# Performance work log

Hardware: AMD Instinct MI355X
Metric: run time of the kernel (lower is better)

The kernel has to match this reference:

```python
import jax, jax.numpy as jnp
import numpy as np

D_MODEL = 1024
NUM_HEADS = 16
D_K = D_MODEL // NUM_HEADS
THETA = 10000.0
B, S = 4, 2048


def apply_rope(x, positions):
    # x: [b, h, s, d_k]; positions: [b, s] int. Interleaved-pair RoPE (cs336 style).
    half = D_K // 2
    inv_freq = THETA ** (-jnp.arange(half, dtype=jnp.float32) * 2.0 / D_K)  # [half]
    ang = positions.astype(jnp.float32)[..., None] * inv_freq  # [b, s, half]
    cos = jnp.cos(ang)[:, None, :, :]  # [b, 1, s, half]
    sin = jnp.sin(ang)[:, None, :, :]
    x_even = x[..., 0::2]
    x_odd = x[..., 1::2]
    r_even = x_even * cos - x_odd * sin
    r_odd = x_even * sin + x_odd * cos
    out = jnp.stack([r_even, r_odd], axis=-1)  # [b,h,s,half,2]
    return out.reshape(x.shape)


def setup_inputs() -> dict:
    key = jax.random.key(0)
    ks = jax.random.split(key, 5)
    scale = 1.0 / np.sqrt(D_MODEL)
    x = jax.random.normal(ks[0], (B, S, D_MODEL), dtype=jnp.float32)
    Qw = jax.random.normal(ks[1], (D_MODEL, D_MODEL), dtype=jnp.float32) * scale
    Kw = jax.random.normal(ks[2], (D_MODEL, D_MODEL), dtype=jnp.float32) * scale
    Vw = jax.random.normal(ks[3], (D_MODEL, D_MODEL), dtype=jnp.float32) * scale
    Ow = jax.random.normal(ks[4], (D_MODEL, D_MODEL), dtype=jnp.float32) * scale
    token_positions = jnp.broadcast_to(jnp.arange(S, dtype=jnp.int32), (B, S))
    return {"x": x, "token_positions": token_positions, "Qw": Qw, "Kw": Kw, "Vw": Vw, "Ow": Ow}


def reference(x, token_positions, Qw, Kw, Vw, Ow):
    b, s, _ = x.shape
    # Projections: einsum('da db, ...sdb -> ...sda') == x @ W.T
    q = jnp.einsum('ab,bsb2->bsa', Qw, x, optimize=True) if False else x @ Qw.T
    k = x @ Kw.T
    v = x @ Vw.T
    # split heads: [b, s, h*dk] -> [b, h, s, dk]
    def split(t):
        return t.reshape(b, s, NUM_HEADS, D_K).transpose(0, 2, 1, 3)
    q, k, v = split(q), split(k), split(v)
    q = apply_rope(q, token_positions)
    k = apply_rope(k, token_positions)
    scores = jnp.einsum('bhqd,bhkd->bhqk', q, k) / jnp.sqrt(jnp.float32(D_K))
    causal = jnp.tril(jnp.ones((s, s), dtype=bool))  # triu(...).T == tril
    scores = jnp.where(causal, scores, jnp.float32(-1e30))
    attn = jax.nn.softmax(scores, axis=-1)
    out = jnp.einsum('bhqk,bhkd->bhqd', attn, v)
    out = out.transpose(0, 2, 1, 3).reshape(b, s, D_MODEL)
    return out @ Ow.T
```

## Files before the change

kernel.cpp:

```cpp
#include <hip/hip_runtime.h>

typedef __attribute__((ext_vector_type(4))) float f32x4;
typedef __attribute__((ext_vector_type(8))) short short8;
typedef __attribute__((ext_vector_type(2))) unsigned short ushort2v;
typedef __attribute__((ext_vector_type(4))) unsigned short ushort4v;

#define D_MODEL 1024
#define NH 16
#define DK 64
#define BSZ 4
#define SSZ 2048
#define M_TOT (BSZ * SSZ)

__device__ __forceinline__ unsigned short f2bf(float f) {
  unsigned int u = __float_as_uint(f);
  u = (u + 0x7FFFu + ((u >> 16) & 1u)) >> 16;
  return (unsigned short)u;
}
__device__ __forceinline__ float bf2f(unsigned short h) {
  return __uint_as_float(((unsigned int)h) << 16);
}
__device__ __forceinline__ unsigned int pk_bf16(float lo, float hi) {
  unsigned int r;
  asm("v_cvt_pk_bf16_f32 %0, %1, %2" : "=v"(r) : "v"(lo), "v"(hi));
  return r;
}
__device__ __forceinline__ float fast_exp2(float x) {
  float r;
  asm("v_exp_f32 %0, %1" : "=v"(r) : "v"(x));
  return r;
}

__global__ void convert_kernel(const float* __restrict__ x,
                               const float* __restrict__ Qw,
                               const float* __restrict__ Kw,
                               const float* __restrict__ Vw,
                               const float* __restrict__ Ow,
                               unsigned short* __restrict__ xb,
                               unsigned short* __restrict__ wqkv,
                               unsigned short* __restrict__ owb) {
  const int NX = M_TOT * D_MODEL;
  const int NO = D_MODEL * D_MODEL;
  const int NW = 3 * NO;
  int idx = (blockIdx.x * blockDim.x + threadIdx.x) * 4;
  const float* src;
  unsigned short* dst;
  if (idx < NX) {
    src = x + idx; dst = xb + idx;
  } else if (idx < NX + NW) {
    int j = idx - NX;
    dst = wqkv + j;
    if (j < NO)            src = Qw + j;
    else if (j < 2 * NO)   src = Kw + (j - NO);
    else                   src = Vw + (j - 2 * NO);
  } else {
    int j = idx - NX - NW;
    src = Ow + j; dst = owb + j;
  }
  float4 v = *(const float4*)src;
  ushort4v o;
  o.x = f2bf(v.x); o.y = f2bf(v.y); o.z = f2bf(v.z); o.w = f2bf(v.w);
  *(ushort4v*)dst = o;
}

template <int MODE>
__global__ __launch_bounds__(256) void gemm_kernel(const unsigned short* __restrict__ A,
                                                   const unsigned short* __restrict__ Bm,
                                                   unsigned short* __restrict__ oQ,
                                                   unsigned short* __restrict__ oK,
                                                   unsigned short* __restrict__ oV,
                                                   float* __restrict__ oF) {
  __shared__ unsigned short As[128 * 32];
  __shared__ unsigned short Bs[128 * 32];
  const int t = threadIdx.x;
  const int lane = t & 63, wave = t >> 6;
  const int l15 = lane & 15, g = lane >> 4;
  const int wr = wave >> 1, wc = wave & 1;
  const int brow = blockIdx.x * 128;
  const int bcol = blockIdx.y * 128;
  const int rA = t >> 2, c8 = (t & 3) * 8;

  f32x4 acc[4][4] = {};

  for (int k0 = 0; k0 < 1024; k0 += 32) {
    __syncthreads();
#pragma unroll
    for (int i = 0; i < 2; ++i) {
      const unsigned short* sa = A + (size_t)(brow + rA + 64 * i) * 1024 + k0 + c8;
      __builtin_amdgcn_global_load_lds((const __attribute__((address_space(1))) void*)sa,
                                       (__attribute__((address_space(3))) void*)(&As[(t + 256 * i) * 8]),
                                       16, 0, 0);
      const unsigned short* sb = Bm + (size_t)(bcol + rA + 64 * i) * 1024 + k0 + c8;
      __builtin_amdgcn_global_load_lds((const __attribute__((address_space(1))) void*)sb,
                                       (__attribute__((address_space(3))) void*)(&Bs[(t + 256 * i) * 8]),
                                       16, 0, 0);
    }
    __syncthreads();
    short8 a[4], b[4];
#pragma unroll
    for (int m = 0; m < 4; ++m)
      a[m] = *(const short8*)(&As[(wr * 64 + m * 16 + l15) * 32 + g * 8]);
#pragma unroll
    for (int n = 0; n < 4; ++n)
      b[n] = *(const short8*)(&Bs[(wc * 64 + n * 16 + l15) * 32 + g * 8]);
#pragma unroll
    for (int m = 0; m < 4; ++m)
#pragma unroll
      for (int n = 0; n < 4; ++n)
        acc[m][n] = __builtin_amdgcn_mfma_f32_16x16x32_bf16(a[m], b[n], acc[m][n], 0, 0, 0);
  }

  const int mbase = brow + wr * 64;
  const int nbase = bcol + wc * 64;
  if (MODE == 0) {
    const int which = bcol >> 10;
#pragma unroll
    for (int m = 0; m < 4; ++m) {
#pragma unroll
      for (int n = 0; n < 4; ++n) {
#pragma unroll
        for (int r = 0; r < 4; ++r) {
          int mrow = mbase + m * 16 + g * 4 + r;
          int ncol = nbase + n * 16 + l15;
          int b = mrow >> 11, s = mrow & 2047;
          int rem = ncol & 1023;
          int h = rem >> 6, d = rem & 63;
          int bh = b * NH + h;
          unsigned short val = f2bf(acc[m][n][r]);
          if (which == 0)      oQ[((size_t)bh * SSZ + s) * DK + d] = val;
          else if (which == 1) oK[((size_t)bh * SSZ + s) * DK + d] = val;
          else                 oV[((size_t)bh * DK + d) * SSZ + s] = val;
        }
      }
    }
  } else {
#pragma unroll
    for (int m = 0; m < 4; ++m) {
#pragma unroll
      for (int n = 0; n < 4; ++n) {
#pragma unroll
        for (int r = 0; r < 4; ++r) {
          int mrow = mbase + m * 16 + g * 4 + r;
          int ncol = nbase + n * 16 + l15;
          oF[(size_t)mrow * D_MODEL + ncol] = acc[m][n][r];
        }
      }
    }
  }
}

__global__ void rope_kernel(unsigned short* __restrict__ Qb,
                            unsigned short* __restrict__ Kb,
                            const int* __restrict__ pos) {
  int idx = blockIdx.x * blockDim.x + threadIdx.x;
  int i = idx & 31;
  int s = (idx >> 5) & (SSZ - 1);
  int bh = idx >> 16;
  int b = bh >> 4;
  float p = (float)pos[b * SSZ + s];
  const float KC = 0.28782313662425572f;
  float invf = expf(-KC * (float)i);
  float ang = p * invf;
  float sn, cs;
  sincosf(ang, &sn, &cs);
  size_t off = ((size_t)bh * SSZ + s) * DK + 2 * i;

  const float QS = 0.18033688011112042f;
  ushort2v q = *(ushort2v*)(Qb + off);
  float qe = bf2f(q.x), qo = bf2f(q.y);
  float re = (qe * cs - qo * sn) * QS;
  float ro = (qe * sn + qo * cs) * QS;
  q.x = f2bf(re); q.y = f2bf(ro);
  *(ushort2v*)(Qb + off) = q;

  ushort2v k = *(ushort2v*)(Kb + off);
  float ke = bf2f(k.x), ko = bf2f(k.y);
  float rke = ke * cs - ko * sn;
  float rko = ke * sn + ko * cs;
  k.x = f2bf(rke); k.y = f2bf(rko);
  *(ushort2v*)(Kb + off) = k;
}

__global__ __launch_bounds__(512) void attn_kernel(const unsigned short* __restrict__ Qb,
                                                   const unsigned short* __restrict__ Kb,
                                                   const unsigned short* __restrict__ Vt,
                                                   unsigned short* __restrict__ Ob) {
  __shared__ unsigned short KS[2][4096];
  __shared__ unsigned short VS[2][4096];
  __shared__ unsigned short PL[8 * 1024];
  const int id = blockIdx.x;
  const int xcd = id & 7, j = id >> 3;
  const int bh = 8 * xcd + (j & 7);
  const int bx = j >> 3;
  const int t = threadIdx.x;
  const int lane = t & 63, wave = t >> 6;
  const int l15 = lane & 15, g = lane >> 4;
  const size_t bhS = (size_t)bh * SSZ;
  char* plb = (char*)PL + wave * 2048;
  const int swz = (l15 & 7) << 4;
  const int b = bh >> 4, h = bh & 15;

  const int sr = t >> 3, ss = (t & 7) ^ (sr & 7);
  auto stage = [&](int bb, int j0) {
    const unsigned short* ks = Kb + (bhS + j0 + sr) * DK + ss * 8;
    __builtin_amdgcn_global_load_lds((const __attribute__((address_space(1))) void*)ks,
                                     (__attribute__((address_space(3))) void*)(&KS[bb][t * 8]),
                                     16, 0, 0);
    const unsigned short* vs = Vt + ((size_t)bh * DK + sr) * SSZ + j0 + ss * 8;
    __builtin_amdgcn_global_load_lds((const __attribute__((address_space(1))) void*)vs,
                                     (__attribute__((address_space(3))) void*)(&VS[bb][t * 8]),
                                     16, 0, 0);
  };

#pragma unroll 1
  for (int half = 0; half < 2; ++half) {
    const int qt = half ? (15 - bx) : bx;
    const int qw0 = qt * 128 + wave * 16;
    short8 qf[2];
#pragma unroll
    for (int ds = 0; ds < 2; ++ds)
      qf[ds] = *(const short8*)(Qb + (bhS + qw0 + l15) * DK + ds * 32 + g * 8);

    f32x4 acc[4] = {};
    float mrun = -3.0e38f, lrun = 0.f;
    const int njt = 2 * (qt + 1);

    int cur = 0;
    stage(0, 0);
    __syncthreads();

#pragma unroll 1
    for (int jt = 0; jt < njt; ++jt) {
      const int j0 = jt * 64;
      if (jt + 1 < njt) stage(cur ^ 1, j0 + 64);

      const unsigned short* Kc = KS[cur];
      short8 kf[4][2];
#pragma unroll
      for (int c = 0; c < 4; ++c)
#pragma unroll
        for (int ds = 0; ds < 2; ++ds)
          kf[c][ds] = *(const short8*)(Kc + (c * 16 + l15) * 64 + (((ds * 4 + g) ^ (l15 & 7)) * 8));

      f32x4 st[4] = {};
#pragma unroll
      for (int c = 0; c < 4; ++c)
#pragma unroll
        for (int ds = 0; ds < 2; ++ds)
          st[c] = __builtin_amdgcn_mfma_f32_16x16x32_bf16(kf[c][ds], qf[ds], st[c], 0, 0, 0);

      if (j0 + 64 > qw0) {
        const int qrow = qw0 + l15;
#pragma unroll
        for (int c = 0; c < 4; ++c) {
          const int kbse = j0 + c * 16 + g * 4;
#pragma unroll
          for (int r = 0; r < 4; ++r)
            if (kbse + r > qrow) st[c][r] = -3.0e38f;
        }
      }

      float mc[4];
#pragma unroll
      for (int c = 0; c < 4; ++c)
        mc[c] = fmaxf(fmaxf(st[c][0], st[c][1]), fmaxf(st[c][2], st[c][3]));
      float pmax = fmaxf(fmaxf(mc[0], mc[1]), fmaxf(mc[2], mc[3]));

      if (!__all(pmax <= mrun + 8.0f)) {
        float mx = fmaxf(pmax, __shfl_xor(pmax, 16));
        mx = fmaxf(mx, __shfl_xor(mx, 32));
        const float mnew = fmaxf(mrun, mx);
        const float corr = fast_exp2(mrun - mnew);
        mrun = mnew;
        lrun *= corr;
#pragma unroll
        for (int n = 0; n < 4; ++n)
#pragma unroll
          for (int r = 0; r < 4; ++r) acc[n][r] *= corr;
      }

      float sc_[4];
#pragma unroll
      for (int c = 0; c < 4; ++c) {
#pragma unroll
        for (int r = 0; r < 4; ++r)
          st[c][r] = fast_exp2(st[c][r] - mrun);
        sc_[c] = (st[c][0] + st[c][1]) + (st[c][2] + st[c][3]);
      }
      lrun += (sc_[0] + sc_[1]) + (sc_[2] + sc_[3]);

#pragma unroll
      for (int c = 0; c < 4; ++c) {
        uint2 ww;
        ww.x = pk_bf16(st[c][0], st[c][1]);
        ww.y = pk_bf16(st[c][2], st[c][3]);
        *(uint2*)(plb + ((l15 * 128 + c * 32 + g * 8) ^ swz)) = ww;
      }
      asm volatile("s_waitcnt lgkmcnt(0)" ::: "memory");
      __builtin_amdgcn_sched_barrier(0);
      short8 pf[2];
#pragma unroll
      for (int d2 = 0; d2 < 2; ++d2)
        pf[d2] = *(const short8*)(plb + ((l15 * 128 + d2 * 64 + g * 16) ^ swz));

      const unsigned short* Vc = VS[cur];
#pragma unroll
      for (int n = 0; n < 4; ++n) {
#pragma unroll
        for (int d2 = 0; d2 < 2; ++d2) {
          short8 vf = *(const short8*)(Vc + (n * 16 + l15) * 64 + (((d2 * 4 + g) ^ (l15 & 7)) * 8));
          acc[n] = __builtin_amdgcn_mfma_f32_16x16x32_bf16(vf, pf[d2], acc[n], 0, 0, 0);
        }
      }

      __syncthreads();
      cur ^= 1;
    }

    lrun += __shfl_xor(lrun, 16);
    lrun += __shfl_xor(lrun, 32);
    const float inv = 1.f / lrun;
    const size_t base = ((size_t)b * SSZ + qw0 + l15) * D_MODEL + h * DK;
#pragma unroll
    for (int n = 0; n < 4; ++n) {
      uint2 ww;
      ww.x = pk_bf16(acc[n][0] * inv, acc[n][1] * inv);
      ww.y = pk_bf16(acc[n][2] * inv, acc[n][3] * inv);
      *(uint2*)((char*)(Ob + base + n * 16 + g * 4)) = ww;
    }
    __syncthreads();
  }
}

extern "C" void kernel_launch(void* const* d_in, const int* in_sizes, int n_in,
                              void* d_out, int out_size, void* d_ws, size_t ws_size,
                              hipStream_t stream) {
  const float* x  = (const float*)d_in[0];
  const int* pos  = (const int*)d_in[1];
  const float* Qw = (const float*)d_in[2];
  const float* Kw = (const float*)d_in[3];
  const float* Vw = (const float*)d_in[4];
  const float* Ow = (const float*)d_in[5];
  float* out = (float*)d_out;

  unsigned short* xb   = (unsigned short*)d_ws;
  unsigned short* wqkv = xb + (size_t)M_TOT * D_MODEL;
  unsigned short* owb  = wqkv + (size_t)3 * D_MODEL * D_MODEL;
  unsigned short* Qb   = owb + (size_t)D_MODEL * D_MODEL;
  unsigned short* Kb   = Qb + (size_t)64 * SSZ * DK;
  unsigned short* Vt   = Kb + (size_t)64 * SSZ * DK;
  unsigned short* Ob   = Vt + (size_t)64 * SSZ * DK;

  {
    int total = M_TOT * D_MODEL + 4 * D_MODEL * D_MODEL;
    convert_kernel<<<total / 4 / 256, 256, 0, stream>>>(x, Qw, Kw, Vw, Ow, xb, wqkv, owb);
  }
  gemm_kernel<0><<<dim3(M_TOT / 128, 3072 / 128), 256, 0, stream>>>(xb, wqkv, Qb, Kb, Vt, nullptr);
  rope_kernel<<<(64 * SSZ * 32) / 256, 256, 0, stream>>>(Qb, Kb, pos);
  attn_kernel<<<512, 512, 0, stream>>>(Qb, Kb, Vt, Ob);
  gemm_kernel<1><<<dim3(M_TOT / 128, D_MODEL / 128), 256, 0, stream>>>(Ob, owb, nullptr, nullptr, nullptr, out);
}
```

Measured before the change: 280.8 us.

## Swizzle GEMM LDS tiles and stage V transpose through LDS for coalesced stores

Applies an XOR swizzle to the 16-byte chunk placement in the A/B LDS tiles, so that MFMA operand reads by lanes in the same wave fall in different banks. For the V output of the QKV projection, which is stored transposed, each wave now packs bf16 pairs into a swizzled LDS scratch region reused from the A/B tiles and writes 16-byte vector stores along the sequence dimension. Before this, the kernel issued scattered 2-byte strided global stores. This adds extra LDS traffic and waits in the epilogue, and it depends on the swizzle index math being consistent between writes and reads.

```diff
diff --git a/kernel.cpp b/kernel.cpp
--- a/kernel.cpp
+++ b/kernel.cpp
@@ -78,7 +78,9 @@
   const int wr = wave >> 1, wc = wave & 1;
   const int brow = blockIdx.x * 128;
   const int bcol = blockIdx.y * 128;
-  const int rA = t >> 2, c8 = (t & 3) * 8;
+  const int rA = t >> 2;
+  const int sq = (t & 3) ^ ((rA >> 1) & 3);
+  const int rseg = ((l15 >> 1) & 3);
 
   f32x4 acc[4][4] = {};
 
@@ -86,11 +88,11 @@
     __syncthreads();
 #pragma unroll
     for (int i = 0; i < 2; ++i) {
-      const unsigned short* sa = A + (size_t)(brow + rA + 64 * i) * 1024 + k0 + c8;
+      const unsigned short* sa = A + (size_t)(brow + rA + 64 * i) * 1024 + k0 + sq * 8;
       __builtin_amdgcn_global_load_lds((const __attribute__((address_space(1))) void*)sa,
                                        (__attribute__((address_space(3))) void*)(&As[(t + 256 * i) * 8]),
                                        16, 0, 0);
-      const unsigned short* sb = Bm + (size_t)(bcol + rA + 64 * i) * 1024 + k0 + c8;
+      const unsigned short* sb = Bm + (size_t)(bcol + rA + 64 * i) * 1024 + k0 + sq * 8;
       __builtin_amdgcn_global_load_lds((const __attribute__((address_space(1))) void*)sb,
                                        (__attribute__((address_space(3))) void*)(&Bs[(t + 256 * i) * 8]),
                                        16, 0, 0);
@@ -99,10 +101,10 @@
     short8 a[4], b[4];
 #pragma unroll
     for (int m = 0; m < 4; ++m)
-      a[m] = *(const short8*)(&As[(wr * 64 + m * 16 + l15) * 32 + g * 8]);
+      a[m] = *(const short8*)(&As[(wr * 64 + m * 16 + l15) * 32 + ((g ^ rseg) * 8)]);
 #pragma unroll
     for (int n = 0; n < 4; ++n)
-      b[n] = *(const short8*)(&Bs[(wc * 64 + n * 16 + l15) * 32 + g * 8]);
+      b[n] = *(const short8*)(&Bs[(wc * 64 + n * 16 + l15) * 32 + ((g ^ rseg) * 8)]);
 #pragma unroll
     for (int m = 0; m < 4; ++m)
 #pragma unroll
@@ -114,23 +116,62 @@
   const int nbase = bcol + wc * 64;
   if (MODE == 0) {
     const int which = bcol >> 10;
-#pragma unroll
-    for (int m = 0; m < 4; ++m) {
-#pragma unroll
-      for (int n = 0; n < 4; ++n) {
-#pragma unroll
-        for (int r = 0; r < 4; ++r) {
-          int mrow = mbase + m * 16 + g * 4 + r;
-          int ncol = nbase + n * 16 + l15;
-          int b = mrow >> 11, s = mrow & 2047;
-          int rem = ncol & 1023;
-          int h = rem >> 6, d = rem & 63;
-          int bh = b * NH + h;
-          unsigned short val = f2bf(acc[m][n][r]);
-          if (which == 0)      oQ[((size_t)bh * SSZ + s) * DK + d] = val;
-          else if (which == 1) oK[((size_t)bh * SSZ + s) * DK + d] = val;
-          else                 oV[((size_t)bh * DK + d) * SSZ + s] = val;
-        }
+    if (which < 2) {
+#pragma unroll
+      for (int m = 0; m < 4; ++m) {
+#pragma unroll
+        for (int n = 0; n < 4; ++n) {
+#pragma unroll
+          for (int r = 0; r < 4; ++r) {
+            int mrow = mbase + m * 16 + g * 4 + r;
+            int ncol = nbase + n * 16 + l15;
+            int b = mrow >> 11, s = mrow & 2047;
+            int rem = ncol & 1023;
+            int h = rem >> 6, d = rem & 63;
+            int bh = b * NH + h;
+            unsigned short val = f2bf(acc[m][n][r]);
+            if (which == 0) oQ[((size_t)bh * SSZ + s) * DK + d] = val;
+            else            oK[((size_t)bh * SSZ + s) * DK + d] = val;
+          }
+        }
+      }
+    } else {
+      __syncthreads();
+      unsigned int* tb = (unsigned int*)(wave < 2 ? (void*)&As[wave * 2048]
+                                                  : (void*)&Bs[(wave - 2) * 2048]);
+      const int bb = mbase >> 11;
+      const int s0 = mbase & 2047;
+      const int hh = ((nbase - 2048) >> 6) & 15;
+#pragma unroll
+      for (int n2 = 0; n2 < 2; ++n2) {
+#pragma unroll
+        for (int nn = 0; nn < 2; ++nn) {
+          const int n = n2 * 2 + nn;
+          const int dloc = nn * 16 + l15;
+          const int xr = (dloc & 7) << 2;
+#pragma unroll
+          for (int m = 0; m < 4; ++m)
+#pragma unroll
+            for (int k = 0; k < 2; ++k) {
+              const int spair = m * 8 + g * 2 + k;
+              unsigned int v = (unsigned)f2bf(acc[m][n][2 * k]) |
+                               ((unsigned)f2bf(acc[m][n][2 * k + 1]) << 16);
+              tb[dloc * 32 + (spair ^ xr)] = v;
+            }
+        }
+        asm volatile("s_waitcnt lgkmcnt(0)" ::: "memory");
+        __builtin_amdgcn_sched_barrier(0);
+        const int dl = lane >> 1, sh = lane & 1;
+        const int xr2 = (dl & 7) << 2;
+        const int dglob = n2 * 32 + dl;
+        unsigned short* vrow = oV + ((size_t)(bb * NH + hh) * DK + dglob) * SSZ + s0;
+#pragma unroll
+        for (int k4 = 0; k4 < 4; ++k4) {
+          uint4 vv = *(const uint4*)&tb[dl * 32 + ((sh * 16 + k4 * 4) ^ xr2)];
+          *(uint4*)(vrow + sh * 32 + k4 * 8) = vv;
+        }
+        asm volatile("s_waitcnt lgkmcnt(0)" ::: "memory");
+        __builtin_amdgcn_sched_barrier(0);
       }
     }
   } else {
```

Measured after the change: 318.5 us. 1.13x slower.
